# Optimization experiments

Measured on AMD Instinct MI355X. Metric: run time of the kernel, lower is better.

Reference implementation:

```python
import jax, jax.numpy as jnp
import numpy as np

B, D, C = 512, 256, 100000
M, S, T = 0.2, 30.0, 1.0
EPS = 1e-12


def _l2norm(x, axis):
    n = jnp.sqrt(jnp.sum(x * x, axis=axis, keepdims=True))
    return x / jnp.maximum(n, EPS)


def setup_inputs() -> dict:
    key = jax.random.key(0)
    ks = jax.random.split(key, 7)
    inputs = jax.random.normal(ks[0], (B, D, 1), dtype=jnp.float32)
    weight = 0.01 * jax.random.normal(ks[1], (C, D), dtype=jnp.float32)
    lam = jax.random.uniform(ks[2], (), dtype=jnp.float32)
    targets1 = jax.random.randint(ks[3], (B,), 0, C)
    pre1 = jax.random.randint(ks[4], (B,), 0, C)
    targets2 = jax.random.randint(ks[5], (B,), 0, C)
    pre2 = jax.random.randint(ks[6], (B,), 0, C)
    return {"inputs": inputs, "weight": weight, "lam": lam,
            "targets1": targets1, "pre1": pre1,
            "targets2": targets2, "pre2": pre2}


def reference(inputs, weight, lam, targets1, pre1, targets2, pre2):
    # inputs: [B, D, 1] -> squeeze frame dim
    x = _l2norm(inputs[:, :, 0], axis=1)          # [B, D]
    w = _l2norm(weight, axis=1)                   # [C, D]
    cos = jnp.einsum('bd,cd->bc', x, w)           # [B, C] cosine similarities
    rows = jnp.arange(B)

    # AM-softmax penalty (lambda_factor = 0 -> penalty = cos - m)
    pen_t1 = cos[rows, targets1] - M
    pen_p1 = cos[rows, pre1] - M
    pen_t2 = cos[rows, targets2] - M
    pen_p2 = cos[rows, pre2] - M

    # Faithful to torch source: targets1 penalty scattered BEFORE scaling by s,
    # the other three scattered AFTER (hence unscaled), same overwrite order.
    out = S * cos.at[rows, targets1].set(pen_t1)
    out = out.at[rows, pre1].set(pen_p1)
    out = out.at[rows, targets2].set(pen_t2)
    out = out.at[rows, pre2].set(pen_p2)

    lsm = jax.nn.log_softmax(out / T, axis=1)     # [B, C]
    ce = lambda tgt: -jnp.mean(lsm[rows, tgt])
    loss = lam * (0.2 * ce(targets1) + 0.8 * ce(pre1)) \
         + (1.0 - lam) * (0.2 * ce(targets2) + 0.8 * ce(pre2))
    return loss
```

## Files before the change

kernel.cpp:

```cpp
#include <hip/hip_runtime.h>
#include <stdint.h>

#define DDIM 256
#define BROWS 512
#define CCOLS 100000
#define NBLK 782
#define NCH  (NBLK * 4)
#define MM 0.2f
#define SS 30.0f

typedef __attribute__((ext_vector_type(8))) short bf16x8;
typedef __attribute__((ext_vector_type(16))) float f32x16;

__device__ __forceinline__ float b2f(unsigned short u) {
    union { unsigned int i; float f; } v; v.i = ((unsigned int)u) << 16; return v.f;
}
__device__ __forceinline__ unsigned short f2b(float f) {
    union { float f; unsigned int i; } v; v.f = f;
    unsigned int r = v.i + 0x7FFFu + ((v.i >> 16) & 1u);
    return (unsigned short)(r >> 16);
}

__global__ void norm_x_pack(const float* __restrict__ x, unsigned short* __restrict__ xp) {
    int row = blockIdx.x * 4 + (threadIdx.x >> 6);
    int ln  = threadIdx.x & 63;
    float4 v = ((const float4*)(x + (size_t)row * DDIM))[ln];
    float ss = v.x * v.x + v.y * v.y + v.z * v.z + v.w * v.w;
#pragma unroll
    for (int m = 1; m <= 32; m <<= 1) ss += __shfl_xor(ss, m);
    float inv = 1.0f / fmaxf(sqrtf(ss), 1e-12f);
    int g = row >> 5, n = row & 31;
    int kk = ln >> 2, hi = (ln >> 1) & 1;
    size_t uoff = ((size_t)(g * 16 + kk) * 64 + hi * 32 + n) * 8 + (ln & 1) * 4;
    ushort4 o;
    o.x = f2b(v.x * inv); o.y = f2b(v.y * inv); o.z = f2b(v.z * inv); o.w = f2b(v.w * inv);
    *(ushort4*)(xp + uoff) = o;
}

__global__ __launch_bounds__(512, 2) void fused_gemm(const float* __restrict__ w,
                                                     const unsigned short* __restrict__ xp,
                                                     float* __restrict__ sums) {
    __shared__ unsigned short wlds[16 * 2 * 128 * 8];
    int blk = blockIdx.x, t = threadIdx.x;
    int cbase = blk * 128;

    {
        int col = t >> 2, q = t & 3;
        int gcol = cbase + col;
        float f[64];
        if (gcol < CCOLS) {
            const float4* src = (const float4*)(w + (size_t)gcol * DDIM + q * 64);
#pragma unroll
            for (int i = 0; i < 16; ++i) {
                float4 v = src[i];
                f[i * 4 + 0] = v.x; f[i * 4 + 1] = v.y; f[i * 4 + 2] = v.z; f[i * 4 + 3] = v.w;
            }
        } else {
#pragma unroll
            for (int i = 0; i < 64; ++i) f[i] = 0.0f;
        }
        float ss = 0.0f;
#pragma unroll
        for (int i = 0; i < 64; ++i) ss += f[i] * f[i];
        ss += __shfl_xor(ss, 1); ss += __shfl_xor(ss, 2);
        float inv = 1.0f / fmaxf(sqrtf(ss), 1e-12f);
#pragma unroll
        for (int s = 0; s < 8; ++s) {
            int kk = q * 4 + (s >> 1), hi = s & 1;
            int o = (s >> 1) * 16 + (s & 1) * 8;
            unsigned int u0 = (unsigned)f2b(f[o+0]*inv) | ((unsigned)f2b(f[o+1]*inv) << 16);
            unsigned int u1 = (unsigned)f2b(f[o+2]*inv) | ((unsigned)f2b(f[o+3]*inv) << 16);
            unsigned int u2 = (unsigned)f2b(f[o+4]*inv) | ((unsigned)f2b(f[o+5]*inv) << 16);
            unsigned int u3 = (unsigned)f2b(f[o+6]*inv) | ((unsigned)f2b(f[o+7]*inv) << 16);
            uint4 pk = make_uint4(u0, u1, u2, u3);
            *(uint4*)(wlds + (size_t)((kk * 2 + hi) * 128 + col) * 8) = pk;
        }
    }
    __syncthreads();

    int wv = t >> 6, lane = t & 63;
    int rg = wv >> 2, cg = wv & 3;
    int m = lane & 31, hi = lane >> 5;

    f32x16 acc[8];
#pragma unroll
    for (int rs = 0; rs < 8; ++rs)
#pragma unroll
        for (int i = 0; i < 16; ++i) acc[rs][i] = 0.0f;

#pragma unroll 4
    for (int kk = 0; kk < 16; ++kk) {
        bf16x8 wf = *(const bf16x8*)(wlds + (size_t)((kk * 2 + hi) * 128 + cg * 32 + m) * 8);
#pragma unroll
        for (int rs = 0; rs < 8; ++rs) {
            bf16x8 xf = *(const bf16x8*)(xp + ((size_t)((rg * 8 + rs) * 16 + kk) * 64 + lane) * 8);
            acc[rs] = __builtin_amdgcn_mfma_f32_32x32x16_bf16(wf, xf, acc[rs], 0, 0, 0);
        }
    }

    int colb = cbase + cg * 32;
#pragma unroll
    for (int rs = 0; rs < 8; ++rs) {
        float p = 0.0f;
#pragma unroll
        for (int r = 0; r < 16; ++r) {
            int cl = (r & 3) + 8 * (r >> 2) + 4 * hi;
            float e = __expf(SS * acc[rs][r]);
            p += (colb + cl < CCOLS) ? e : 0.0f;
        }
        p += __shfl_xor(p, 32);
        if (hi == 0) {
            int row = rg * 256 + rs * 32 + m;
            sums[(size_t)row * NCH + blk * 4 + cg] = p;
        }
    }
}

__global__ void reduce_finalize(const float* __restrict__ sums,
                                const float* __restrict__ x, const float* __restrict__ w,
                                const float* __restrict__ lamp,
                                const int* __restrict__ t1, const int* __restrict__ p1,
                                const int* __restrict__ t2, const int* __restrict__ p2,
                                float* __restrict__ out) {
    int b = blockIdx.x, t = threadIdx.x;
    float s = 0.0f;
    for (int i = t; i < NCH; i += 256) s += sums[(size_t)b * NCH + i];
#pragma unroll
    for (int m = 1; m <= 32; m <<= 1) s += __shfl_xor(s, m);
    __shared__ float ls[4];
    if ((t & 63) == 0) ls[t >> 6] = s;
    __syncthreads();
    if (t < 64) {
        int ln = t;
        float rowsum = ls[0] + ls[1] + ls[2] + ls[3];
        float4 xv = ((const float4*)(x + (size_t)b * DDIM))[ln];
        float ssx = xv.x*xv.x + xv.y*xv.y + xv.z*xv.z + xv.w*xv.w;
#pragma unroll
        for (int m = 1; m <= 32; m <<= 1) ssx += __shfl_xor(ssx, m);
        float xinv = 1.0f / fmaxf(sqrtf(ssx), 1e-12f);
        int idx[4] = { t1[b], p1[b], t2[b], p2[b] };
        float cosv[4];
#pragma unroll
        for (int k = 0; k < 4; ++k) {
            float4 wv = ((const float4*)(w + (size_t)idx[k] * DDIM))[ln];
            float d  = xv.x*wv.x + xv.y*wv.y + xv.z*wv.z + xv.w*wv.w;
            float sw = wv.x*wv.x + wv.y*wv.y + wv.z*wv.z + wv.w*wv.w;
#pragma unroll
            for (int m = 1; m <= 32; m <<= 1) { d += __shfl_xor(d, m); sw += __shfl_xor(sw, m); }
            cosv[k] = d * xinv / fmaxf(sqrtf(sw), 1e-12f);
        }
        if (ln == 0) {
            auto finalv = [&](int k) -> float {
                int c = idx[k]; float cv = cosv[k];
                if (c == idx[3]) return cv - MM;
                if (c == idx[2]) return cv - MM;
                if (c == idx[1]) return cv - MM;
                return SS * (cv - MM);
            };
            float delta = 0.0f;
#pragma unroll
            for (int k = 0; k < 4; ++k) {
                bool first = true;
                for (int j = 0; j < k; ++j) if (idx[j] == idx[k]) first = false;
                if (first) delta += __expf(finalv(k)) - __expf(SS * cosv[k]);
            }
            float lse = logf(rowsum + delta);
            float lam = lamp[0];
            float lossb = lam          * (0.2f * (lse - finalv(0)) + 0.8f * (lse - finalv(1)))
                        + (1.0f - lam) * (0.2f * (lse - finalv(2)) + 0.8f * (lse - finalv(3)));
            atomicAdd(out, lossb * (1.0f / 512.0f));
        }
    }
}

extern "C" void kernel_launch(void* const* d_in, const int* in_sizes, int n_in,
                              void* d_out, int out_size, void* d_ws, size_t ws_size,
                              hipStream_t stream) {
    const float* x   = (const float*)d_in[0];
    const float* w   = (const float*)d_in[1];
    const float* lam = (const float*)d_in[2];
    const int* t1    = (const int*)d_in[3];
    const int* p1    = (const int*)d_in[4];
    const int* t2    = (const int*)d_in[5];
    const int* p2    = (const int*)d_in[6];
    float* out = (float*)d_out;

    char* ws = (char*)d_ws;
    unsigned short* xpack = (unsigned short*)ws;
    float* sums = (float*)(ws + 262144);

    hipMemsetAsync(out, 0, sizeof(float), stream);
    norm_x_pack<<<128, 256, 0, stream>>>(x, xpack);
    fused_gemm<<<NBLK, 512, 0, stream>>>(w, xpack, sums);
    reduce_finalize<<<BROWS, 256, 0, stream>>>(sums, x, w, lam, t1, p1, t2, p2, out);
}
```

Measured before the change: 305.5 us.

## Pre-pack normalized weights to bf16 and split GEMM over row groups with atomic row sums

Result: faster. 277.8 us (-9.1%).

```diff
diff --git a/kernel.cpp b/kernel.cpp
--- a/kernel.cpp
+++ b/kernel.cpp
@@ -4,17 +4,15 @@
 #define DDIM 256
 #define BROWS 512
 #define CCOLS 100000
-#define NBLK 782
-#define NCH  (NBLK * 4)
+#define CGRP 3125
+#define CGRP_PAD 3128
+#define NBLKC 782
 #define MM 0.2f
 #define SS 30.0f
 
 typedef __attribute__((ext_vector_type(8))) short bf16x8;
 typedef __attribute__((ext_vector_type(16))) float f32x16;
 
-__device__ __forceinline__ float b2f(unsigned short u) {
-    union { unsigned int i; float f; } v; v.i = ((unsigned int)u) << 16; return v.f;
-}
 __device__ __forceinline__ unsigned short f2b(float f) {
     union { float f; unsigned int i; } v; v.f = f;
     unsigned int r = v.i + 0x7FFFu + ((v.i >> 16) & 1u);
@@ -23,84 +21,76 @@
 
 __global__ void norm_x_pack(const float* __restrict__ x, unsigned short* __restrict__ xp) {
     int row = blockIdx.x * 4 + (threadIdx.x >> 6);
-    int ln  = threadIdx.x & 63;
-    float4 v = ((const float4*)(x + (size_t)row * DDIM))[ln];
-    float ss = v.x * v.x + v.y * v.y + v.z * v.z + v.w * v.w;
+    int l   = threadIdx.x & 63;
+    float4 v = ((const float4*)(x + (size_t)row * DDIM))[l];
+    float ss = v.x*v.x + v.y*v.y + v.z*v.z + v.w*v.w;
 #pragma unroll
     for (int m = 1; m <= 32; m <<= 1) ss += __shfl_xor(ss, m);
     float inv = 1.0f / fmaxf(sqrtf(ss), 1e-12f);
     int g = row >> 5, n = row & 31;
-    int kk = ln >> 2, hi = (ln >> 1) & 1;
-    size_t uoff = ((size_t)(g * 16 + kk) * 64 + hi * 32 + n) * 8 + (ln & 1) * 4;
+    int kk = l >> 2, hi = (l >> 1) & 1;
+    size_t uoff = ((size_t)(g * 16 + kk) * 64 + hi * 32 + n) * 8 + (l & 1) * 4;
     ushort4 o;
-    o.x = f2b(v.x * inv); o.y = f2b(v.y * inv); o.z = f2b(v.z * inv); o.w = f2b(v.w * inv);
+    o.x = f2b(v.x*inv); o.y = f2b(v.y*inv); o.z = f2b(v.z*inv); o.w = f2b(v.w*inv);
     *(ushort4*)(xp + uoff) = o;
 }
 
-__global__ __launch_bounds__(512, 2) void fused_gemm(const float* __restrict__ w,
-                                                     const unsigned short* __restrict__ xp,
-                                                     float* __restrict__ sums) {
-    __shared__ unsigned short wlds[16 * 2 * 128 * 8];
-    int blk = blockIdx.x, t = threadIdx.x;
-    int cbase = blk * 128;
-
-    {
-        int col = t >> 2, q = t & 3;
-        int gcol = cbase + col;
-        float f[64];
-        if (gcol < CCOLS) {
-            const float4* src = (const float4*)(w + (size_t)gcol * DDIM + q * 64);
+__global__ __launch_bounds__(256) void norm_w_pack(const float* __restrict__ w,
+                                                   unsigned short* __restrict__ wp) {
+    __shared__ unsigned short wlds[8192];
+    int blk = blockIdx.x;
+    int t = threadIdx.x, wv = t >> 6, l = t & 63;
+    const float* wb = w + (size_t)blk * 32 * DDIM;
+    int kk = l >> 2, hi = (l >> 1) & 1;
 #pragma unroll
-            for (int i = 0; i < 16; ++i) {
-                float4 v = src[i];
-                f[i * 4 + 0] = v.x; f[i * 4 + 1] = v.y; f[i * 4 + 2] = v.z; f[i * 4 + 3] = v.w;
-            }
-        } else {
+    for (int i = 0; i < 8; ++i) {
+        int c = i * 4 + wv;
+        float4 v = *(const float4*)(wb + (size_t)c * DDIM + 4 * l);
+        float ss = v.x*v.x + v.y*v.y + v.z*v.z + v.w*v.w;
 #pragma unroll
-            for (int i = 0; i < 64; ++i) f[i] = 0.0f;
-        }
-        float ss = 0.0f;
-#pragma unroll
-        for (int i = 0; i < 64; ++i) ss += f[i] * f[i];
-        ss += __shfl_xor(ss, 1); ss += __shfl_xor(ss, 2);
+        for (int m = 1; m <= 32; m <<= 1) ss += __shfl_xor(ss, m);
         float inv = 1.0f / fmaxf(sqrtf(ss), 1e-12f);
-#pragma unroll
-        for (int s = 0; s < 8; ++s) {
-            int kk = q * 4 + (s >> 1), hi = s & 1;
-            int o = (s >> 1) * 16 + (s & 1) * 8;
-            unsigned int u0 = (unsigned)f2b(f[o+0]*inv) | ((unsigned)f2b(f[o+1]*inv) << 16);
-            unsigned int u1 = (unsigned)f2b(f[o+2]*inv) | ((unsigned)f2b(f[o+3]*inv) << 16);
-            unsigned int u2 = (unsigned)f2b(f[o+4]*inv) | ((unsigned)f2b(f[o+5]*inv) << 16);
-            unsigned int u3 = (unsigned)f2b(f[o+6]*inv) | ((unsigned)f2b(f[o+7]*inv) << 16);
-            uint4 pk = make_uint4(u0, u1, u2, u3);
-            *(uint4*)(wlds + (size_t)((kk * 2 + hi) * 128 + col) * 8) = pk;
-        }
+        ushort4 o;
+        o.x = f2b(v.x*inv); o.y = f2b(v.y*inv); o.z = f2b(v.z*inv); o.w = f2b(v.w*inv);
+        *(ushort4*)(wlds + ((size_t)((kk * 2 + hi) * 32 + c)) * 8 + (l & 1) * 4) = o;
     }
     __syncthreads();
+    const uint4* src = (const uint4*)wlds;
+    uint4* dst = (uint4*)(wp + (size_t)blk * 8192);
+#pragma unroll
+    for (int j = 0; j < 4; ++j) dst[j * 256 + t] = src[j * 256 + t];
+}
 
-    int wv = t >> 6, lane = t & 63;
-    int rg = wv >> 2, cg = wv & 3;
+__global__ __launch_bounds__(256, 3) void gemm_lse(const unsigned short* __restrict__ wp,
+                                                   const unsigned short* __restrict__ xp,
+                                                   float* __restrict__ rowacc) {
+    __shared__ float red[4][128];
+    int blkc = blockIdx.x, rgrp = blockIdx.y;
+    int t = threadIdx.x, cg = t >> 6, lane = t & 63;
     int m = lane & 31, hi = lane >> 5;
 
-    f32x16 acc[8];
+    const unsigned short* wbase = wp + (size_t)(blkc * 4 + cg) * 8192 + lane * 8;
+    const unsigned short* xbase = xp + (size_t)(rgrp * 4) * 8192 + lane * 8;
+
+    f32x16 acc[4];
 #pragma unroll
-    for (int rs = 0; rs < 8; ++rs)
+    for (int rs = 0; rs < 4; ++rs)
 #pragma unroll
         for (int i = 0; i < 16; ++i) acc[rs][i] = 0.0f;
 
-#pragma unroll 4
+#pragma unroll
     for (int kk = 0; kk < 16; ++kk) {
-        bf16x8 wf = *(const bf16x8*)(wlds + (size_t)((kk * 2 + hi) * 128 + cg * 32 + m) * 8);
+        bf16x8 wf = *(const bf16x8*)(wbase + kk * 512);
 #pragma unroll
-        for (int rs = 0; rs < 8; ++rs) {
-            bf16x8 xf = *(const bf16x8*)(xp + ((size_t)((rg * 8 + rs) * 16 + kk) * 64 + lane) * 8);
+        for (int rs = 0; rs < 4; ++rs) {
+            bf16x8 xf = *(const bf16x8*)(xbase + rs * 8192 + kk * 512);
             acc[rs] = __builtin_amdgcn_mfma_f32_32x32x16_bf16(wf, xf, acc[rs], 0, 0, 0);
         }
     }
 
-    int colb = cbase + cg * 32;
+    int colb = blkc * 128 + cg * 32;
 #pragma unroll
-    for (int rs = 0; rs < 8; ++rs) {
+    for (int rs = 0; rs < 4; ++rs) {
         float p = 0.0f;
 #pragma unroll
         for (int r = 0; r < 16; ++r) {
@@ -109,67 +99,59 @@
             p += (colb + cl < CCOLS) ? e : 0.0f;
         }
         p += __shfl_xor(p, 32);
-        if (hi == 0) {
-            int row = rg * 256 + rs * 32 + m;
-            sums[(size_t)row * NCH + blk * 4 + cg] = p;
-        }
+        if (hi == 0) red[cg][rs * 32 + m] = p;
+    }
+    __syncthreads();
+    if (t < 128) {
+        float s = red[0][t] + red[1][t] + red[2][t] + red[3][t];
+        atomicAdd(&rowacc[rgrp * 128 + t], s);
     }
 }
 
-__global__ void reduce_finalize(const float* __restrict__ sums,
-                                const float* __restrict__ x, const float* __restrict__ w,
-                                const float* __restrict__ lamp,
-                                const int* __restrict__ t1, const int* __restrict__ p1,
-                                const int* __restrict__ t2, const int* __restrict__ p2,
-                                float* __restrict__ out) {
-    int b = blockIdx.x, t = threadIdx.x;
-    float s = 0.0f;
-    for (int i = t; i < NCH; i += 256) s += sums[(size_t)b * NCH + i];
+__global__ void finalize(const float* __restrict__ rowacc,
+                         const float* __restrict__ x, const float* __restrict__ w,
+                         const float* __restrict__ lamp,
+                         const int* __restrict__ t1, const int* __restrict__ p1,
+                         const int* __restrict__ t2, const int* __restrict__ p2,
+                         float* __restrict__ out) {
+    int b  = blockIdx.x * 4 + (threadIdx.x >> 6);
+    int ln = threadIdx.x & 63;
+    float4 xv = ((const float4*)(x + (size_t)b * DDIM))[ln];
+    float ssx = xv.x*xv.x + xv.y*xv.y + xv.z*xv.z + xv.w*xv.w;
 #pragma unroll
-    for (int m = 1; m <= 32; m <<= 1) s += __shfl_xor(s, m);
-    __shared__ float ls[4];
-    if ((t & 63) == 0) ls[t >> 6] = s;
-    __syncthreads();
-    if (t < 64) {
-        int ln = t;
-        float rowsum = ls[0] + ls[1] + ls[2] + ls[3];
-        float4 xv = ((const float4*)(x + (size_t)b * DDIM))[ln];
-        float ssx = xv.x*xv.x + xv.y*xv.y + xv.z*xv.z + xv.w*xv.w;
+    for (int m = 1; m <= 32; m <<= 1) ssx += __shfl_xor(ssx, m);
+    float xinv = 1.0f / fmaxf(sqrtf(ssx), 1e-12f);
+    int idx[4] = { t1[b], p1[b], t2[b], p2[b] };
+    float cosv[4];
 #pragma unroll
-        for (int m = 1; m <= 32; m <<= 1) ssx += __shfl_xor(ssx, m);
-        float xinv = 1.0f / fmaxf(sqrtf(ssx), 1e-12f);
-        int idx[4] = { t1[b], p1[b], t2[b], p2[b] };
-        float cosv[4];
+    for (int k = 0; k < 4; ++k) {
+        float4 wv = ((const float4*)(w + (size_t)idx[k] * DDIM))[ln];
+        float d  = xv.x*wv.x + xv.y*wv.y + xv.z*wv.z + xv.w*wv.w;
+        float sw = wv.x*wv.x + wv.y*wv.y + wv.z*wv.z + wv.w*wv.w;
+#pragma unroll
+        for (int m = 1; m <= 32; m <<= 1) { d += __shfl_xor(d, m); sw += __shfl_xor(sw, m); }
+        cosv[k] = d * xinv / fmaxf(sqrtf(sw), 1e-12f);
+    }
+    if (ln == 0) {
+        auto finalv = [&](int k) -> float {
+            int c = idx[k]; float cv = cosv[k];
+            if (c == idx[3]) return cv - MM;
+            if (c == idx[2]) return cv - MM;
+            if (c == idx[1]) return cv - MM;
+            return SS * (cv - MM);
+        };
+        float delta = 0.0f;
 #pragma unroll
         for (int k = 0; k < 4; ++k) {
-            float4 wv = ((const float4*)(w + (size_t)idx[k] * DDIM))[ln];
-            float d  = xv.x*wv.x + xv.y*wv.y + xv.z*wv.z + xv.w*wv.w;
-            float sw = wv.x*wv.x + wv.y*wv.y + wv.z*wv.z + wv.w*wv.w;
-#pragma unroll
-            for (int m = 1; m <= 32; m <<= 1) { d += __shfl_xor(d, m); sw += __shfl_xor(sw, m); }
-            cosv[k] = d * xinv / fmaxf(sqrtf(sw), 1e-12f);
+            bool first = true;
+            for (int j = 0; j < k; ++j) if (idx[j] == idx[k]) first = false;
+            if (first) delta += __expf(finalv(k)) - __expf(SS * cosv[k]);
         }
-        if (ln == 0) {
-            auto finalv = [&](int k) -> float {
-                int c = idx[k]; float cv = cosv[k];
-                if (c == idx[3]) return cv - MM;
-                if (c == idx[2]) return cv - MM;
-                if (c == idx[1]) return cv - MM;
-                return SS * (cv - MM);
-            };
-            float delta = 0.0f;
-#pragma unroll
-            for (int k = 0; k < 4; ++k) {
-                bool first = true;
-                for (int j = 0; j < k; ++j) if (idx[j] == idx[k]) first = false;
-                if (first) delta += __expf(finalv(k)) - __expf(SS * cosv[k]);
-            }
-            float lse = logf(rowsum + delta);
-            float lam = lamp[0];
-            float lossb = lam          * (0.2f * (lse - finalv(0)) + 0.8f * (lse - finalv(1)))
-                        + (1.0f - lam) * (0.2f * (lse - finalv(2)) + 0.8f * (lse - finalv(3)));
-            atomicAdd(out, lossb * (1.0f / 512.0f));
-        }
+        float lse = logf(rowacc[b] + delta);
+        float lam = lamp[0];
+        float lossb = lam          * (0.2f * (lse - finalv(0)) + 0.8f * (lse - finalv(1)))
+                    + (1.0f - lam) * (0.2f * (lse - finalv(2)) + 0.8f * (lse - finalv(3)));
+        atomicAdd(out, lossb * (1.0f / 512.0f));
     }
 }
 
@@ -187,10 +169,15 @@
 
     char* ws = (char*)d_ws;
     unsigned short* xpack = (unsigned short*)ws;
-    float* sums = (float*)(ws + 262144);
+    unsigned short* wpack = (unsigned short*)(ws + 262144);
+    float* rowacc = (float*)(ws + 262144 + 51249152);
 
     hipMemsetAsync(out, 0, sizeof(float), stream);
+    hipMemsetAsync(rowacc, 0, BROWS * sizeof(float), stream);
+    hipMemsetAsync((char*)wpack + (size_t)CGRP * 16384, 0, (CGRP_PAD - CGRP) * 16384, stream);
+
     norm_x_pack<<<128, 256, 0, stream>>>(x, xpack);
-    fused_gemm<<<NBLK, 512, 0, stream>>>(w, xpack, sums);
-    reduce_finalize<<<BROWS, 256, 0, stream>>>(sums, x, w, lam, t1, p1, t2, p2, out);
+    norm_w_pack<<<CGRP, 256, 0, stream>>>(w, wpack);
+    gemm_lse<<<dim3(NBLKC, 4), 256, 0, stream>>>(wpack, xpack, rowacc);
+    finalize<<<128, 256, 0, stream>>>(rowacc, x, w, lam, t1, p1, t2, p2, out);
 }
```
